# Kernel tuning notes

Hardware: AMD Instinct MI355X
Metric: run time of the kernel (lower is better)

## Reference

```python
import jax, jax.numpy as jnp
import numpy as np

DIM = 256
NUM_HEADS = 8
HEAD_DIM = DIM // NUM_HEADS


def setup_inputs() -> dict:
    key = jax.random.key(0)
    k_x, k_wq, k_bq, k_wp, k_bp = jax.random.split(key, 5)
    B, C, H, W = 2, DIM, 48, 48
    x = jax.random.normal(k_x, (B, C, H, W), dtype=jnp.float32)
    # 1x1 convs are pointwise matmuls: store weights as [out, in]
    w_qkv = jax.random.normal(k_wq, (3 * C, C), dtype=jnp.float32) * (1.0 / np.sqrt(C))
    b_qkv = jax.random.normal(k_bq, (3 * C,), dtype=jnp.float32) * 0.01
    w_proj = jax.random.normal(k_wp, (C, C), dtype=jnp.float32) * (1.0 / np.sqrt(C))
    b_proj = jax.random.normal(k_bp, (C,), dtype=jnp.float32) * 0.01
    return {"x": x, "w_qkv": w_qkv, "b_qkv": b_qkv, "w_proj": w_proj, "b_proj": b_proj}


def reference(x, w_qkv, b_qkv, w_proj, b_proj):
    B, C, H, W = x.shape
    N = H * W
    # qkv 1x1 conv -> pointwise channel matmul
    qkv = jnp.einsum('bchw,oc->bohw', x, w_qkv) + b_qkv[None, :, None, None]
    q, k, v = jnp.split(qkv, 3, axis=1)  # each [B, C, H, W]
    q = q.reshape(B, NUM_HEADS, HEAD_DIM, N)
    k = k.reshape(B, NUM_HEADS, HEAD_DIM, N)
    v = v.reshape(B, NUM_HEADS, HEAD_DIM, N)
    scale = 1.0 / (HEAD_DIM ** 0.5)
    attn = jnp.einsum('bhdn,bhdm->bhnm', q, k) * scale  # [B, H, N, N]
    attn = jax.nn.softmax(attn, axis=-1)
    out = jnp.einsum('bhnm,bhdm->bhdn', attn, v)  # [B, heads, head_dim, N]
    out = out.reshape(B, C, H, W)
    out = jnp.einsum('bchw,oc->bohw', out, w_proj) + b_proj[None, :, None, None]
    return out + x
```

## Files before the change

kernel.cpp:

```cpp
#include <hip/hip_runtime.h>
#include <math.h>

#define C_DIM 256
#define NH 8
#define HD 32
#define BATCH 2
#define NPIX 2304
#define TK 64
#define NGRP (NPIX / 16)
#define TPB 18

typedef __attribute__((ext_vector_type(8))) short bf16x8;
typedef __attribute__((ext_vector_type(4))) float f32x4;

#define OFF_XT  0u
#define OFF_Q   1179648u
#define OFF_K   2359296u
#define OFF_V   3538944u
#define OFF_OT  4718592u
#define OFF_WQ  5898240u
#define OFF_WP  6094848u
#define OFF_F32 6160384u

__device__ __forceinline__ unsigned short f2b(float f) {
    union { float f; unsigned int u; } c; c.f = f;
    unsigned int u = c.u + 0x7FFFu + ((c.u >> 16) & 1u);
    return (unsigned short)(u >> 16);
}
__device__ __forceinline__ unsigned int pk2(float lo, float hi) {
    union { float f; unsigned int u; } a, b;
    a.f = lo; b.f = hi;
    return __builtin_amdgcn_perm(b.u + 0x8000u, a.u + 0x8000u, 0x07060302u);
}
__device__ __forceinline__ unsigned int cvtpk(float lo, float hi) {
    unsigned int r;
    asm("v_cvt_pk_bf16_f32 %0, %1, %2" : "=v"(r) : "v"(lo), "v"(hi));
    return r;
}
__device__ __forceinline__ float fexp2(float x) {
#if __has_builtin(__builtin_amdgcn_exp2f)
    return __builtin_amdgcn_exp2f(x);
#else
    return exp2f(x);
#endif
}

__global__ __launch_bounds__(256) void prep_all(
        const float* __restrict__ x, unsigned short* __restrict__ xT,
        const float* __restrict__ wqkv, const float* __restrict__ wproj,
        unsigned short* __restrict__ wq, unsigned short* __restrict__ wp)
{
    __shared__ unsigned short t_s[64][72];
    const int bid = blockIdx.x;
    const int tid = threadIdx.x;
    if (bid < 288) {
        const int bx = bid % 36, by = (bid / 36) & 3, bz = bid / 144;
        const int n0 = bx * 64, c0 = by * 64, b = bz;
        const int nl = tid & 63, cq = tid >> 6;
        #pragma unroll
        for (int p = 0; p < 8; ++p) {
            const int c = p * 8 + cq * 2;
            const float f0 = x[((size_t)b * C_DIM + c0 + c) * NPIX + n0 + nl];
            const float f1 = x[((size_t)b * C_DIM + c0 + c + 1) * NPIX + n0 + nl];
            *(unsigned int*)&t_s[nl][c] = pk2(f0, f1);
        }
        __syncthreads();
        const int row = tid >> 2, jq = tid & 3;
        #pragma unroll
        for (int hh = 0; hh < 2; ++hh) {
            const int jl = jq * 2 + hh;
            const int jg = by * 8 + jl;
            const int ngrp = bx * 4 + (row >> 4);
            unsigned short* dst = xT + (((size_t)b * NGRP + ngrp) * 32 + jg) * 128 + (row & 15) * 8;
            *(uint4*)dst = *(uint4*)&t_s[row][jl * 8];
        }
    } else {
        const int t = (bid - 288) * 256 + tid;
        const float* src; unsigned short* dst;
        if (t < 24576) {
            const int m = t >> 5, j = t & 31;
            src = wqkv + ((size_t)m * C_DIM + j * 8);
            dst = wq + ((size_t)((m >> 4) * 32 + j) * 16 + (m & 15)) * 8;
        } else {
            const int t2 = t - 24576, m = t2 >> 5, j = t2 & 31;
            src = wproj + ((size_t)m * C_DIM + j * 8);
            dst = wp + ((size_t)((m >> 4) * 32 + j) * 16 + (m & 15)) * 8;
        }
        const float4 f0 = *(const float4*)src, f1 = *(const float4*)(src + 4);
        *(uint4*)dst = make_uint4(pk2(f0.x, f0.y), pk2(f0.z, f0.w),
                                  pk2(f1.x, f1.y), pk2(f1.z, f1.w));
    }
}

__global__ __launch_bounds__(256, 2) void qkv_gemm(
        const unsigned short* __restrict__ xT, const unsigned short* __restrict__ wq,
        const float* __restrict__ bias,
        unsigned short* __restrict__ Qg, unsigned short* __restrict__ Kg,
        unsigned short* __restrict__ Vg)
{
    __shared__ unsigned short eplds[4][2560];
    const int tid = threadIdx.x, wv = tid >> 6, lane = tid & 63;
    const int l15 = lane & 15, quad = lane >> 4;
    const int n0 = blockIdx.x * 256, my = blockIdx.y, b = blockIdx.z;
    const int nw = n0 + wv * 64;

    bf16x8 af[2][8];
    #pragma unroll
    for (int mt = 0; mt < 2; ++mt)
        #pragma unroll
        for (int kc = 0; kc < 8; ++kc)
            af[mt][kc] = *(const bf16x8*)(wq +
                ((size_t)((my * 2 + mt) * 32 + kc * 4 + quad) * 16 + l15) * 8);

    f32x4 acc[2][4];
    #pragma unroll
    for (int mt = 0; mt < 2; ++mt)
        #pragma unroll
        for (int s = 0; s < 4; ++s) acc[mt][s] = (f32x4){0.f, 0.f, 0.f, 0.f};

    #pragma unroll
    for (int sub = 0; sub < 4; ++sub) {
        const int ngrp = (nw + sub * 16) >> 4;
        const unsigned short* bp = xT + ((size_t)b * NGRP + ngrp) * 32 * 128;
        #pragma unroll
        for (int kc = 0; kc < 8; ++kc) {
            const bf16x8 bf = *(const bf16x8*)(bp + (size_t)(kc * 4 + quad) * 128 + l15 * 8);
            acc[0][sub] = __builtin_amdgcn_mfma_f32_16x16x32_bf16(af[0][kc], bf, acc[0][sub], 0, 0, 0);
            acc[1][sub] = __builtin_amdgcn_mfma_f32_16x16x32_bf16(af[1][kc], bf, acc[1][sub], 0, 0, 0);
        }
    }

    const int which = my >> 3;
    const int h = my & 7, bh = b * NH + h;
    float4 b4[2];
    b4[0] = *(const float4*)(bias + my * 32 + quad * 4);
    b4[1] = *(const float4*)(bias + my * 32 + 16 + quad * 4);
    unsigned short* wl = eplds[wv];

    if (which < 2) {
        const float sc = (which == 0) ? 0.2550348576f : 1.0f;
        #pragma unroll
        for (int mt = 0; mt < 2; ++mt)
            #pragma unroll
            for (int sub = 0; sub < 4; ++sub) {
                const float v0 = (acc[mt][sub][0] + b4[mt].x) * sc;
                const float v1 = (acc[mt][sub][1] + b4[mt].y) * sc;
                const float v2 = (acc[mt][sub][2] + b4[mt].z) * sc;
                const float v3 = (acc[mt][sub][3] + b4[mt].w) * sc;
                *(uint2*)&wl[(sub * 16 + l15) * 40 + mt * 16 + quad * 4] =
                    make_uint2(pk2(v0, v1), pk2(v2, v3));
            }
        unsigned short* dst = ((which == 0) ? Qg : Kg)
                            + ((size_t)bh * NPIX + nw + lane) * HD;
        #pragma unroll
        for (int i = 0; i < 4; ++i)
            *((uint4*)dst + i) = *(uint4*)&wl[lane * 40 + i * 8];
    } else {
        #pragma unroll
        for (int mt = 0; mt < 2; ++mt)
            #pragma unroll
            for (int sub = 0; sub < 4; ++sub) {
                wl[(mt * 16 + quad * 4 + 0) * 72 + sub * 16 + l15] = f2b(acc[mt][sub][0] + b4[mt].x);
                wl[(mt * 16 + quad * 4 + 1) * 72 + sub * 16 + l15] = f2b(acc[mt][sub][1] + b4[mt].y);
                wl[(mt * 16 + quad * 4 + 2) * 72 + sub * 16 + l15] = f2b(acc[mt][sub][2] + b4[mt].z);
                wl[(mt * 16 + quad * 4 + 3) * 72 + sub * 16 + l15] = f2b(acc[mt][sub][3] + b4[mt].w);
            }
        const int row = lane >> 1, seg = (lane & 1) * 32;
        unsigned short* dst = Vg + ((size_t)bh * HD + row) * NPIX + nw + seg;
        #pragma unroll
        for (int i = 0; i < 4; ++i)
            *((uint4*)dst + i) = *(uint4*)&wl[row * 72 + seg + i * 8];
    }
}

__global__ __launch_bounds__(256, 4) void attn_kernel(
        const unsigned short* __restrict__ Qg, const unsigned short* __restrict__ Kg,
        const unsigned short* __restrict__ Vg,
        float* __restrict__ OtP, float* __restrict__ lsumP)
{
    __shared__ unsigned short k_s[2][TK][40];
    __shared__ unsigned short v_s[2][HD][76];
    __shared__ float ep_s[4][16][36];

    const int tid  = threadIdx.x;
    const int wv   = tid >> 6;
    const int lane = tid & 63;
    const int l15  = lane & 15;
    const int quad = lane >> 4;
    const int bh   = blockIdx.x;
    const int q0   = blockIdx.y * 64;
    const int sp   = blockIdx.z;
    const int t0   = sp * TPB;

    const unsigned short* Qh = Qg + (size_t)bh * NPIX * HD;
    const unsigned short* Kh = Kg + (size_t)bh * NPIX * HD;
    const unsigned short* Vh = Vg + (size_t)bh * HD * NPIX;

    const bf16x8 q_frag = *(const bf16x8*)(Qh + (size_t)(q0 + wv * 16 + l15) * HD + quad * 8);
    const bf16x8 onesf = {16256, 16256, 16256, 16256, 16256, 16256, 16256, 16256};

    const int kr = tid >> 2, kc = (tid & 3) * 8;
    const int ksl = (kr & 0x23) | ((kr & 0x04) << 2) | ((kr & 0x18) >> 1);
    const int vd = tid >> 3, vc = (tid & 7) * 8;

    uint4 kreg = *(const uint4*)(Kh + (size_t)(t0 * TK + kr) * HD + kc);
    uint4 vreg = *(const uint4*)(Vh + (size_t)vd * NPIX + t0 * TK + vc);
    *(uint4*)&k_s[0][ksl][kc] = kreg;
    *(uint4*)&v_s[0][vd][vc] = vreg;

    f32x4 o0 = {0.f, 0.f, 0.f, 0.f};
    f32x4 o1 = {0.f, 0.f, 0.f, 0.f};
    f32x4 ol = {0.f, 0.f, 0.f, 0.f};

    for (int t = 0; t < TPB; ++t) {
        const int cur = t & 1;
        if (t + 1 < TPB) {
            const int k0 = (t0 + t + 1) * TK;
            kreg = *(const uint4*)(Kh + (size_t)(k0 + kr) * HD + kc);
            vreg = *(const uint4*)(Vh + (size_t)vd * NPIX + k0 + vc);
        }
        __syncthreads();

        f32x4 s[4];
        #pragma unroll
        for (int kg = 0; kg < 4; ++kg) {
            const bf16x8 kf = *(const bf16x8*)&k_s[cur][kg * 16 + l15][quad * 8];
            s[kg] = __builtin_amdgcn_mfma_f32_16x16x32_bf16(kf, q_frag,
                        (f32x4){0.f, 0.f, 0.f, 0.f}, 0, 0, 0);
        }

        bf16x8 pf[2];
        #pragma unroll
        for (int kc2 = 0; kc2 < 2; ++kc2) {
            union { unsigned int u[4]; bf16x8 v; } c;
            c.u[0] = cvtpk(fexp2(s[2 * kc2][0]),     fexp2(s[2 * kc2][1]));
            c.u[1] = cvtpk(fexp2(s[2 * kc2][2]),     fexp2(s[2 * kc2][3]));
            c.u[2] = cvtpk(fexp2(s[2 * kc2 + 1][0]), fexp2(s[2 * kc2 + 1][1]));
            c.u[3] = cvtpk(fexp2(s[2 * kc2 + 1][2]), fexp2(s[2 * kc2 + 1][3]));
            pf[kc2] = c.v;
        }

        #pragma unroll
        for (int kc2 = 0; kc2 < 2; ++kc2) {
            const bf16x8 vf0 = *(const bf16x8*)&v_s[cur][l15][kc2 * 32 + quad * 8];
            const bf16x8 vf1 = *(const bf16x8*)&v_s[cur][16 + l15][kc2 * 32 + quad * 8];
            o0 = __builtin_amdgcn_mfma_f32_16x16x32_bf16(vf0, pf[kc2], o0, 0, 0, 0);
            o1 = __builtin_amdgcn_mfma_f32_16x16x32_bf16(vf1, pf[kc2], o1, 0, 0, 0);
            ol = __builtin_amdgcn_mfma_f32_16x16x32_bf16(onesf, pf[kc2], ol, 0, 0, 0);
        }

        if (t + 1 < TPB) {
            *(uint4*)&k_s[cur ^ 1][ksl][kc] = kreg;
            *(uint4*)&v_s[cur ^ 1][vd][vc] = vreg;
        }
    }

    float* pp = &ep_s[wv][0][0];
    #pragma unroll
    for (int r = 0; r < 4; ++r) {
        pp[l15 * 36 + quad * 4 + r]      = o0[r];
        pp[l15 * 36 + 16 + quad * 4 + r] = o1[r];
    }
    if (quad == 0)
        lsumP[((size_t)sp * 16 + bh) * NPIX + q0 + wv * 16 + l15] = ol[0];
    const int q = lane >> 2, off = (lane & 3) * 8;
    float* dst = OtP + (((size_t)sp * 16 + bh) * NPIX + q0 + wv * 16 + q) * 32 + off;
    *(float4*)dst       = *(float4*)&pp[q * 36 + off];
    *((float4*)dst + 1) = *(float4*)&pp[q * 36 + off + 4];
}

__global__ __launch_bounds__(256) void norm_kernel(
        const float* __restrict__ OtP, const float* __restrict__ lsumP,
        unsigned short* __restrict__ OtT)
{
    const int t = blockIdx.x * 256 + threadIdx.x;
    const int q = t >> 2, jq = t & 3;
    const int bh = blockIdx.y;
    const float* pa = OtP + ((size_t)bh * NPIX + q) * 32 + jq * 8;
    const float* pb = OtP + ((size_t)(16 + bh) * NPIX + q) * 32 + jq * 8;
    const float inv = 1.f / (lsumP[(size_t)bh * NPIX + q] +
                             lsumP[(size_t)(16 + bh) * NPIX + q]);
    const int b = bh >> 3, h = bh & 7;
    unsigned short* cell = OtT + (((size_t)b * NGRP + (q >> 4)) * 32 + h * 4) * 128
                         + (q & 15) * 8 + jq * 128;
    const float4 a0 = *(const float4*)(pa);
    const float4 a1 = *(const float4*)(pa + 4);
    const float4 b0 = *(const float4*)(pb);
    const float4 b1 = *(const float4*)(pb + 4);
    const float o0 = (a0.x + b0.x) * inv, o1 = (a0.y + b0.y) * inv;
    const float o2 = (a0.z + b0.z) * inv, o3 = (a0.w + b0.w) * inv;
    const float o4 = (a1.x + b1.x) * inv, o5 = (a1.y + b1.y) * inv;
    const float o6 = (a1.z + b1.z) * inv, o7 = (a1.w + b1.w) * inv;
    *(uint4*)cell = make_uint4(cvtpk(o0, o1), cvtpk(o2, o3),
                               cvtpk(o4, o5), cvtpk(o6, o7));
}

__global__ __launch_bounds__(256) void proj_gemm(
        const unsigned short* __restrict__ OtT, const unsigned short* __restrict__ wp,
        const float* __restrict__ bias, const float* __restrict__ x,
        float* __restrict__ out)
{
    __shared__ float plds[4][576];
    const int tid = threadIdx.x, wv = tid >> 6, lane = tid & 63;
    const int l15 = lane & 15, quad = lane >> 4;
    const int n0 = blockIdx.x * 128, my = blockIdx.y, b = blockIdx.z;
    const int nw = n0 + wv * 32;

    bf16x8 af[8];
    #pragma unroll
    for (int kc = 0; kc < 8; ++kc)
        af[kc] = *(const bf16x8*)(wp + ((size_t)(my * 32 + kc * 4 + quad) * 16 + l15) * 8);

    f32x4 acc[2];
    acc[0] = (f32x4){0.f, 0.f, 0.f, 0.f};
    acc[1] = (f32x4){0.f, 0.f, 0.f, 0.f};

    #pragma unroll
    for (int sub = 0; sub < 2; ++sub) {
        const int ngrp = (nw + sub * 16) >> 4;
        const unsigned short* bp = OtT + ((size_t)b * NGRP + ngrp) * 32 * 128;
        #pragma unroll
        for (int kc = 0; kc < 8; ++kc) {
            const bf16x8 bf = *(const bf16x8*)(bp + (size_t)(kc * 4 + quad) * 128 + l15 * 8);
            acc[sub] = __builtin_amdgcn_mfma_f32_16x16x32_bf16(af[kc], bf, acc[sub], 0, 0, 0);
        }
    }

    float* wl = plds[wv];
    #pragma unroll
    for (int sub = 0; sub < 2; ++sub) {
        wl[(quad * 4 + 0) * 36 + sub * 16 + l15] = acc[sub][0];
        wl[(quad * 4 + 1) * 36 + sub * 16 + l15] = acc[sub][1];
        wl[(quad * 4 + 2) * 36 + sub * 16 + l15] = acc[sub][2];
        wl[(quad * 4 + 3) * 36 + sub * 16 + l15] = acc[sub][3];
    }
    const int m0 = my * 16;
    #pragma unroll
    for (int p = 0; p < 2; ++p) {
        const int row = p * 8 + (lane >> 3), cn = (lane & 7) * 4;
        const int c = m0 + row;
        const size_t idx = ((size_t)b * C_DIM + c) * NPIX + nw + cn;
        const f32x4 v = *(const f32x4*)&wl[row * 36 + cn];
        const f32x4 r = *(const f32x4*)(x + idx);
        const float bv = bias[c];
        f32x4 o;
        o[0] = v[0] + bv + r[0]; o[1] = v[1] + bv + r[1];
        o[2] = v[2] + bv + r[2]; o[3] = v[3] + bv + r[3];
        *(f32x4*)(out + idx) = o;
    }
}

extern "C" void kernel_launch(void* const* d_in, const int* in_sizes, int n_in,
                              void* d_out, int out_size, void* d_ws, size_t ws_size,
                              hipStream_t stream)
{
    const float* x      = (const float*)d_in[0];
    const float* w_qkv  = (const float*)d_in[1];
    const float* b_qkv  = (const float*)d_in[2];
    const float* w_proj = (const float*)d_in[3];
    const float* b_proj = (const float*)d_in[4];
    float* out = (float*)d_out;

    unsigned short* ws = (unsigned short*)d_ws;
    unsigned short* xT  = ws + OFF_XT;
    unsigned short* Qg  = ws + OFF_Q;
    unsigned short* Kg  = ws + OFF_K;
    unsigned short* Vg  = ws + OFF_V;
    unsigned short* OtT = ws + OFF_OT;
    unsigned short* wq  = ws + OFF_WQ;
    unsigned short* wp  = ws + OFF_WP;
    float* fws   = (float*)(ws + OFF_F32);
    float* OtP   = fws;
    float* lsumP = fws + 4718592;

    prep_all<<<dim3(416), 256, 0, stream>>>(x, xT, w_qkv, w_proj, wq, wp);
    qkv_gemm<<<dim3(9, 24, 2), 256, 0, stream>>>(xT, wq, b_qkv, Qg, Kg, Vg);
    attn_kernel<<<dim3(16, 36, 2), 256, 0, stream>>>(Qg, Kg, Vg, OtP, lsumP);
    norm_kernel<<<dim3(36, 16), 256, 0, stream>>>(OtP, lsumP, OtT);
    proj_gemm<<<dim3(18, 16, 2), 256, 0, stream>>>(OtT, wp, b_proj, x, out);
}
```

Measured before the change: 106.0 us.

## Process two 16-query tiles per wave in attention to reuse K/V fragments

Each wave now handles 32 queries instead of 16, so a block covers 128 queries and the grid's query dimension halves. K and V fragments loaded from shared memory, along with the staged K/V tiles, are reused across two query sub-tiles. This cuts LDS reads and global K/V traffic per unit of work. In exchange it raises register pressure (launch bounds relaxed from 4 to 2 blocks), doubles the epilogue LDS, and halves the number of blocks, which may underfill the GPU.

```diff
diff --git a/kernel.cpp b/kernel.cpp
--- a/kernel.cpp
+++ b/kernel.cpp
@@ -173,14 +173,14 @@
     }
 }
 
-__global__ __launch_bounds__(256, 4) void attn_kernel(
+__global__ __launch_bounds__(256, 2) void attn_kernel(
         const unsigned short* __restrict__ Qg, const unsigned short* __restrict__ Kg,
         const unsigned short* __restrict__ Vg,
         float* __restrict__ OtP, float* __restrict__ lsumP)
 {
     __shared__ unsigned short k_s[2][TK][40];
     __shared__ unsigned short v_s[2][HD][76];
-    __shared__ float ep_s[4][16][36];
+    __shared__ float ep_s[4][32][36];
 
     const int tid  = threadIdx.x;
     const int wv   = tid >> 6;
@@ -188,7 +188,7 @@
     const int l15  = lane & 15;
     const int quad = lane >> 4;
     const int bh   = blockIdx.x;
-    const int q0   = blockIdx.y * 64;
+    const int q0   = blockIdx.y * 128;
     const int sp   = blockIdx.z;
     const int t0   = sp * TPB;
 
@@ -196,7 +196,9 @@
     const unsigned short* Kh = Kg + (size_t)bh * NPIX * HD;
     const unsigned short* Vh = Vg + (size_t)bh * HD * NPIX;
 
-    const bf16x8 q_frag = *(const bf16x8*)(Qh + (size_t)(q0 + wv * 16 + l15) * HD + quad * 8);
+    const int qb = q0 + wv * 32;
+    const bf16x8 qA = *(const bf16x8*)(Qh + (size_t)(qb + l15) * HD + quad * 8);
+    const bf16x8 qB = *(const bf16x8*)(Qh + (size_t)(qb + 16 + l15) * HD + quad * 8);
     const bf16x8 onesf = {16256, 16256, 16256, 16256, 16256, 16256, 16256, 16256};
 
     const int kr = tid >> 2, kc = (tid & 3) * 8;
@@ -208,9 +210,9 @@
     *(uint4*)&k_s[0][ksl][kc] = kreg;
     *(uint4*)&v_s[0][vd][vc] = vreg;
 
-    f32x4 o0 = {0.f, 0.f, 0.f, 0.f};
-    f32x4 o1 = {0.f, 0.f, 0.f, 0.f};
-    f32x4 ol = {0.f, 0.f, 0.f, 0.f};
+    f32x4 oA0 = {0.f, 0.f, 0.f, 0.f}, oA1 = {0.f, 0.f, 0.f, 0.f};
+    f32x4 oB0 = {0.f, 0.f, 0.f, 0.f}, oB1 = {0.f, 0.f, 0.f, 0.f};
+    f32x4 olA = {0.f, 0.f, 0.f, 0.f}, olB = {0.f, 0.f, 0.f, 0.f};
 
     for (int t = 0; t < TPB; ++t) {
         const int cur = t & 1;
@@ -221,32 +223,42 @@
         }
         __syncthreads();
 
-        f32x4 s[4];
+        f32x4 sA[4], sB[4];
         #pragma unroll
         for (int kg = 0; kg < 4; ++kg) {
             const bf16x8 kf = *(const bf16x8*)&k_s[cur][kg * 16 + l15][quad * 8];
-            s[kg] = __builtin_amdgcn_mfma_f32_16x16x32_bf16(kf, q_frag,
+            sA[kg] = __builtin_amdgcn_mfma_f32_16x16x32_bf16(kf, qA,
                         (f32x4){0.f, 0.f, 0.f, 0.f}, 0, 0, 0);
-        }
-
-        bf16x8 pf[2];
+            sB[kg] = __builtin_amdgcn_mfma_f32_16x16x32_bf16(kf, qB,
+                        (f32x4){0.f, 0.f, 0.f, 0.f}, 0, 0, 0);
+        }
+
+        bf16x8 pfA[2], pfB[2];
         #pragma unroll
         for (int kc2 = 0; kc2 < 2; ++kc2) {
-            union { unsigned int u[4]; bf16x8 v; } c;
-            c.u[0] = cvtpk(fexp2(s[2 * kc2][0]),     fexp2(s[2 * kc2][1]));
-            c.u[1] = cvtpk(fexp2(s[2 * kc2][2]),     fexp2(s[2 * kc2][3]));
-            c.u[2] = cvtpk(fexp2(s[2 * kc2 + 1][0]), fexp2(s[2 * kc2 + 1][1]));
-            c.u[3] = cvtpk(fexp2(s[2 * kc2 + 1][2]), fexp2(s[2 * kc2 + 1][3]));
-            pf[kc2] = c.v;
+            union { unsigned int u[4]; bf16x8 v; } cA, cB;
+            cA.u[0] = cvtpk(fexp2(sA[2 * kc2][0]),     fexp2(sA[2 * kc2][1]));
+            cA.u[1] = cvtpk(fexp2(sA[2 * kc2][2]),     fexp2(sA[2 * kc2][3]));
+            cA.u[2] = cvtpk(fexp2(sA[2 * kc2 + 1][0]), fexp2(sA[2 * kc2 + 1][1]));
+            cA.u[3] = cvtpk(fexp2(sA[2 * kc2 + 1][2]), fexp2(sA[2 * kc2 + 1][3]));
+            pfA[kc2] = cA.v;
+            cB.u[0] = cvtpk(fexp2(sB[2 * kc2][0]),     fexp2(sB[2 * kc2][1]));
+            cB.u[1] = cvtpk(fexp2(sB[2 * kc2][2]),     fexp2(sB[2 * kc2][3]));
+            cB.u[2] = cvtpk(fexp2(sB[2 * kc2 + 1][0]), fexp2(sB[2 * kc2 + 1][1]));
+            cB.u[3] = cvtpk(fexp2(sB[2 * kc2 + 1][2]), fexp2(sB[2 * kc2 + 1][3]));
+            pfB[kc2] = cB.v;
         }
 
         #pragma unroll
         for (int kc2 = 0; kc2 < 2; ++kc2) {
             const bf16x8 vf0 = *(const bf16x8*)&v_s[cur][l15][kc2 * 32 + quad * 8];
             const bf16x8 vf1 = *(const bf16x8*)&v_s[cur][16 + l15][kc2 * 32 + quad * 8];
-            o0 = __builtin_amdgcn_mfma_f32_16x16x32_bf16(vf0, pf[kc2], o0, 0, 0, 0);
-            o1 = __builtin_amdgcn_mfma_f32_16x16x32_bf16(vf1, pf[kc2], o1, 0, 0, 0);
-            ol = __builtin_amdgcn_mfma_f32_16x16x32_bf16(onesf, pf[kc2], ol, 0, 0, 0);
+            oA0 = __builtin_amdgcn_mfma_f32_16x16x32_bf16(vf0, pfA[kc2], oA0, 0, 0, 0);
+            oA1 = __builtin_amdgcn_mfma_f32_16x16x32_bf16(vf1, pfA[kc2], oA1, 0, 0, 0);
+            oB0 = __builtin_amdgcn_mfma_f32_16x16x32_bf16(vf0, pfB[kc2], oB0, 0, 0, 0);
+            oB1 = __builtin_amdgcn_mfma_f32_16x16x32_bf16(vf1, pfB[kc2], oB1, 0, 0, 0);
+            olA = __builtin_amdgcn_mfma_f32_16x16x32_bf16(onesf, pfA[kc2], olA, 0, 0, 0);
+            olB = __builtin_amdgcn_mfma_f32_16x16x32_bf16(onesf, pfB[kc2], olB, 0, 0, 0);
         }
 
         if (t + 1 < TPB) {
@@ -258,15 +270,20 @@
     float* pp = &ep_s[wv][0][0];
     #pragma unroll
     for (int r = 0; r < 4; ++r) {
-        pp[l15 * 36 + quad * 4 + r]      = o0[r];
-        pp[l15 * 36 + 16 + quad * 4 + r] = o1[r];
-    }
-    if (quad == 0)
-        lsumP[((size_t)sp * 16 + bh) * NPIX + q0 + wv * 16 + l15] = ol[0];
-    const int q = lane >> 2, off = (lane & 3) * 8;
-    float* dst = OtP + (((size_t)sp * 16 + bh) * NPIX + q0 + wv * 16 + q) * 32 + off;
-    *(float4*)dst       = *(float4*)&pp[q * 36 + off];
-    *((float4*)dst + 1) = *(float4*)&pp[q * 36 + off + 4];
+        pp[l15 * 36 + quad * 4 + r]             = oA0[r];
+        pp[l15 * 36 + 16 + quad * 4 + r]        = oA1[r];
+        pp[(16 + l15) * 36 + quad * 4 + r]      = oB0[r];
+        pp[(16 + l15) * 36 + 16 + quad * 4 + r] = oB1[r];
+    }
+    if (quad == 0) {
+        lsumP[((size_t)sp * 16 + bh) * NPIX + qb + l15]      = olA[0];
+        lsumP[((size_t)sp * 16 + bh) * NPIX + qb + 16 + l15] = olB[0];
+    }
+    const int q = lane >> 1, off = (lane & 1) * 16;
+    float* dst = OtP + (((size_t)sp * 16 + bh) * NPIX + qb + q) * 32 + off;
+    #pragma unroll
+    for (int i = 0; i < 4; ++i)
+        *((float4*)dst + i) = *(float4*)&pp[q * 36 + off + i * 4];
 }
 
 __global__ __launch_bounds__(256) void norm_kernel(
@@ -375,7 +392,7 @@
 
     prep_all<<<dim3(416), 256, 0, stream>>>(x, xT, w_qkv, w_proj, wq, wp);
     qkv_gemm<<<dim3(9, 24, 2), 256, 0, stream>>>(xT, wq, b_qkv, Qg, Kg, Vg);
-    attn_kernel<<<dim3(16, 36, 2), 256, 0, stream>>>(Qg, Kg, Vg, OtP, lsumP);
+    attn_kernel<<<dim3(16, 18, 2), 256, 0, stream>>>(Qg, Kg, Vg, OtP, lsumP);
     norm_kernel<<<dim3(36, 16), 256, 0, stream>>>(OtP, lsumP, OtT);
     proj_gemm<<<dim3(18, 16, 2), 256, 0, stream>>>(OtT, wp, b_proj, x, out);
 }
```

Result: no change. 107.0 us (+0.9%).

## Drop split-K attention and fuse normalization into attention epilogue

Applied to the files above, without the earlier changes.

Removes the two-way key split in the attention kernel so each block processes all key tiles, then normalizes by the row sum and writes bf16 output directly into the projection layout. This eliminates the fp32 partial buffers, the separate norm kernel launch, and the associated global traffic. The trade-off is half as many attention blocks (576 instead of 1152), which lowers parallelism and gives each block a longer serial loop.

```diff
diff --git a/kernel.cpp b/kernel.cpp
--- a/kernel.cpp
+++ b/kernel.cpp
@@ -8,7 +8,7 @@
 #define NPIX 2304
 #define TK 64
 #define NGRP (NPIX / 16)
-#define TPB 18
+#define TPB 36
 
 typedef __attribute__((ext_vector_type(8))) short bf16x8;
 typedef __attribute__((ext_vector_type(4))) float f32x4;
@@ -20,7 +20,6 @@
 #define OFF_OT  4718592u
 #define OFF_WQ  5898240u
 #define OFF_WP  6094848u
-#define OFF_F32 6160384u
 
 __device__ __forceinline__ unsigned short f2b(float f) {
     union { float f; unsigned int u; } c; c.f = f;
@@ -176,11 +175,10 @@
 __global__ __launch_bounds__(256, 4) void attn_kernel(
         const unsigned short* __restrict__ Qg, const unsigned short* __restrict__ Kg,
         const unsigned short* __restrict__ Vg,
-        float* __restrict__ OtP, float* __restrict__ lsumP)
+        unsigned short* __restrict__ OtT)
 {
     __shared__ unsigned short k_s[2][TK][40];
     __shared__ unsigned short v_s[2][HD][76];
-    __shared__ float ep_s[4][16][36];
 
     const int tid  = threadIdx.x;
     const int wv   = tid >> 6;
@@ -189,8 +187,6 @@
     const int quad = lane >> 4;
     const int bh   = blockIdx.x;
     const int q0   = blockIdx.y * 64;
-    const int sp   = blockIdx.z;
-    const int t0   = sp * TPB;
 
     const unsigned short* Qh = Qg + (size_t)bh * NPIX * HD;
     const unsigned short* Kh = Kg + (size_t)bh * NPIX * HD;
@@ -203,8 +199,8 @@
     const int ksl = (kr & 0x23) | ((kr & 0x04) << 2) | ((kr & 0x18) >> 1);
     const int vd = tid >> 3, vc = (tid & 7) * 8;
 
-    uint4 kreg = *(const uint4*)(Kh + (size_t)(t0 * TK + kr) * HD + kc);
-    uint4 vreg = *(const uint4*)(Vh + (size_t)vd * NPIX + t0 * TK + vc);
+    uint4 kreg = *(const uint4*)(Kh + (size_t)kr * HD + kc);
+    uint4 vreg = *(const uint4*)(Vh + (size_t)vd * NPIX + vc);
     *(uint4*)&k_s[0][ksl][kc] = kreg;
     *(uint4*)&v_s[0][vd][vc] = vreg;
 
@@ -215,7 +211,7 @@
     for (int t = 0; t < TPB; ++t) {
         const int cur = t & 1;
         if (t + 1 < TPB) {
-            const int k0 = (t0 + t + 1) * TK;
+            const int k0 = (t + 1) * TK;
             kreg = *(const uint4*)(Kh + (size_t)(k0 + kr) * HD + kc);
             vreg = *(const uint4*)(Vh + (size_t)vd * NPIX + k0 + vc);
         }
@@ -255,44 +251,18 @@
         }
     }
 
-    float* pp = &ep_s[wv][0][0];
-    #pragma unroll
-    for (int r = 0; r < 4; ++r) {
-        pp[l15 * 36 + quad * 4 + r]      = o0[r];
-        pp[l15 * 36 + 16 + quad * 4 + r] = o1[r];
-    }
-    if (quad == 0)
-        lsumP[((size_t)sp * 16 + bh) * NPIX + q0 + wv * 16 + l15] = ol[0];
-    const int q = lane >> 2, off = (lane & 3) * 8;
-    float* dst = OtP + (((size_t)sp * 16 + bh) * NPIX + q0 + wv * 16 + q) * 32 + off;
-    *(float4*)dst       = *(float4*)&pp[q * 36 + off];
-    *((float4*)dst + 1) = *(float4*)&pp[q * 36 + off + 4];
-}
-
-__global__ __launch_bounds__(256) void norm_kernel(
-        const float* __restrict__ OtP, const float* __restrict__ lsumP,
-        unsigned short* __restrict__ OtT)
-{
-    const int t = blockIdx.x * 256 + threadIdx.x;
-    const int q = t >> 2, jq = t & 3;
-    const int bh = blockIdx.y;
-    const float* pa = OtP + ((size_t)bh * NPIX + q) * 32 + jq * 8;
-    const float* pb = OtP + ((size_t)(16 + bh) * NPIX + q) * 32 + jq * 8;
-    const float inv = 1.f / (lsumP[(size_t)bh * NPIX + q] +
-                             lsumP[(size_t)(16 + bh) * NPIX + q]);
+    const float inv = 1.f / ol[0];
     const int b = bh >> 3, h = bh & 7;
-    unsigned short* cell = OtT + (((size_t)b * NGRP + (q >> 4)) * 32 + h * 4) * 128
-                         + (q & 15) * 8 + jq * 128;
-    const float4 a0 = *(const float4*)(pa);
-    const float4 a1 = *(const float4*)(pa + 4);
-    const float4 b0 = *(const float4*)(pb);
-    const float4 b1 = *(const float4*)(pb + 4);
-    const float o0 = (a0.x + b0.x) * inv, o1 = (a0.y + b0.y) * inv;
-    const float o2 = (a0.z + b0.z) * inv, o3 = (a0.w + b0.w) * inv;
-    const float o4 = (a1.x + b1.x) * inv, o5 = (a1.y + b1.y) * inv;
-    const float o6 = (a1.z + b1.z) * inv, o7 = (a1.w + b1.w) * inv;
-    *(uint4*)cell = make_uint4(cvtpk(o0, o1), cvtpk(o2, o3),
-                               cvtpk(o4, o5), cvtpk(o6, o7));
+    const int qg = q0 + wv * 16 + l15;
+    unsigned short* base = OtT + (((size_t)b * NGRP + (qg >> 4)) * 32 + h * 4) * 128
+                         + (qg & 15) * 8;
+    const int jq0 = quad >> 1, half = (quad & 1) * 4;
+    const uint2 w0 = make_uint2(cvtpk(o0[0] * inv, o0[1] * inv),
+                                cvtpk(o0[2] * inv, o0[3] * inv));
+    const uint2 w1 = make_uint2(cvtpk(o1[0] * inv, o1[1] * inv),
+                                cvtpk(o1[2] * inv, o1[3] * inv));
+    *(uint2*)(base + (size_t)jq0 * 128 + half)       = w0;
+    *(uint2*)(base + (size_t)(2 + jq0) * 128 + half) = w1;
 }
 
 __global__ __launch_bounds__(256) void proj_gemm(
@@ -369,13 +339,9 @@
     unsigned short* OtT = ws + OFF_OT;
     unsigned short* wq  = ws + OFF_WQ;
     unsigned short* wp  = ws + OFF_WP;
-    float* fws   = (float*)(ws + OFF_F32);
-    float* OtP   = fws;
-    float* lsumP = fws + 4718592;
 
     prep_all<<<dim3(416), 256, 0, stream>>>(x, xT, w_qkv, w_proj, wq, wp);
     qkv_gemm<<<dim3(9, 24, 2), 256, 0, stream>>>(xT, wq, b_qkv, Qg, Kg, Vg);
-    attn_kernel<<<dim3(16, 36, 2), 256, 0, stream>>>(Qg, Kg, Vg, OtP, lsumP);
-    norm_kernel<<<dim3(36, 16), 256, 0, stream>>>(OtP, lsumP, OtT);
+    attn_kernel<<<dim3(16, 36), 256, 0, stream>>>(Qg, Kg, Vg, OtT);
     proj_gemm<<<dim3(18, 16, 2), 256, 0, stream>>>(OtT, wp, b_proj, x, out);
 }
```

After: 105.9 us. Within noise of the previous version (-0.1%).
